# Performance work log

Measured on AMD Instinct MI355X. Metric: run time of the kernel, lower is better.

Reference implementation:

```python
import jax, jax.numpy as jnp
import numpy as np

KERNEL = 7
PAD = 3


def setup_inputs() -> dict:
    key = jax.random.key(0)
    k1, k2, k3 = jax.random.split(key, 3)
    B, C, H, W = 16, 256, 64, 64
    x = jax.random.normal(k1, (B, C, H, W), dtype=jnp.float32)
    weight = jax.random.normal(k2, (C, KERNEL * KERNEL), dtype=jnp.float32)
    bias = jax.random.normal(k3, (C,), dtype=jnp.float32)
    return {"x": x, "weight": weight, "bias": bias}


def reference(x, weight, bias):
    # x: (B, C, H, W); weight: (C, K*K) laid out row-major as in nn.Unfold
    # (unfold * weight).sum over the K*K patch dim == depthwise 'same' conv.
    C = weight.shape[0]
    kernel = weight.reshape(C, 1, KERNEL, KERNEL)  # OIHW with I=1, groups=C
    out = jax.lax.conv_general_dilated(
        x, kernel,
        window_strides=(1, 1),
        padding=((PAD, PAD), (PAD, PAD)),
        dimension_numbers=("NCHW", "OIHW", "NCHW"),
        feature_group_count=C,
    )
    out = out + bias[None, :, None, None]
    # Original wraps this in to_sparse(): a lossless repacking of nonzero
    # pixels into (indices, features) with data-dependent shape. Its dense()
    # equals `out`, so we return the dense form.
    return out
```

## Files before the change

### kernel.cpp

```cpp
#include <hip/hip_runtime.h>

#define LDSW 80
#define LDSH 70
#define KSZ 7
#define PAD 3

__global__ __launch_bounds__(256, 4)
void dwconv7x7_kernel(const float* __restrict__ x,
                      const float* __restrict__ weight,
                      const float* __restrict__ bias,
                      float* __restrict__ out) {
    __shared__ float tile[LDSH * LDSW];

    const int bc  = blockIdx.x;
    const int c   = bc & 255;
    const int tid = threadIdx.x;

    const float4 z4 = make_float4(0.f, 0.f, 0.f, 0.f);
#pragma unroll
    for (int k = 0; k < 6; ++k) {
        int g = tid + k * 256;
        if (g < (LDSH * LDSW) / 4)
            *reinterpret_cast<float4*>(&tile[g * 4]) = z4;
    }

    const float* wp = weight + c * (KSZ * KSZ);
    float wk[KSZ * KSZ];
#pragma unroll
    for (int k = 0; k < KSZ * KSZ; ++k) wk[k] = wp[k];
    const float bv = bias[c];

    __syncthreads();

    const float* xp = x + (size_t)bc * 4096;
#pragma unroll
    for (int k = 0; k < 4; ++k) {
        int g = tid + k * 256;
        int h = g >> 4;
        int w = (g & 15) * 4;
        float4 v = *reinterpret_cast<const float4*>(&xp[g * 4]);
        *reinterpret_cast<float4*>(&tile[(h + PAD) * LDSW + (w + 4)]) = v;
    }
    __syncthreads();

    const int tx = tid & 15;
    const int ty = tid >> 4;
    const int wb = tx * 4;
    const int hb = ty * 4;

    float acc[4][4];
#pragma unroll
    for (int i = 0; i < 4; ++i)
#pragma unroll
        for (int j = 0; j < 4; ++j) acc[i][j] = 0.f;

#pragma unroll
    for (int r = 0; r < 10; ++r) {
        const float* row = &tile[(hb + r) * LDSW + wb];
        float4 q0 = *reinterpret_cast<const float4*>(row);
        float4 q1 = *reinterpret_cast<const float4*>(row + 4);
        float4 q2 = *reinterpret_cast<const float4*>(row + 8);
        float f[12] = {q0.x, q0.y, q0.z, q0.w,
                       q1.x, q1.y, q1.z, q1.w,
                       q2.x, q2.y, q2.z, q2.w};
#pragma unroll
        for (int i = 0; i < 4; ++i) {
            if (r - i >= 0 && r - i <= 6) {
                const int kr = r - i;
#pragma unroll
                for (int j = 0; j < 4; ++j) {
#pragma unroll
                    for (int kc = 0; kc < KSZ; ++kc) {
                        acc[i][j] += f[j + 1 + kc] * wk[kr * KSZ + kc];
                    }
                }
            }
        }
    }

    float* op = out + (size_t)bc * 4096;
#pragma unroll
    for (int i = 0; i < 4; ++i) {
        float4 v;
        v.x = acc[i][0] + bv;
        v.y = acc[i][1] + bv;
        v.z = acc[i][2] + bv;
        v.w = acc[i][3] + bv;
        *reinterpret_cast<float4*>(&op[(hb + i) * 64 + wb]) = v;
    }
}

extern "C" void kernel_launch(void* const* d_in, const int* in_sizes, int n_in,
                              void* d_out, int out_size, void* d_ws, size_t ws_size,
                              hipStream_t stream) {
    const float* x      = (const float*)d_in[0];
    const float* weight = (const float*)d_in[1];
    const float* bias   = (const float*)d_in[2];
    float* out          = (float*)d_out;
    (void)in_sizes; (void)n_in; (void)out_size; (void)d_ws; (void)ws_size;

    dim3 grid(16 * 256);
    dim3 block(256);
    dwconv7x7_kernel<<<grid, block, 0, stream>>>(x, weight, bias, out);
}
```

Before: 39.31 us.

## Replace LDS tiling with direct global loads into registers per wave

Drops the shared-memory tile, its zero-fill and both barriers. Each wave now handles half a plane, and each thread computes an 8x4 output block by reading 14 input rows straight from global memory with float4 loads and masking the padding in registers. This removes LDS traffic and synchronisation and raises output reuse per thread. In exchange it issues redundant global loads that depend on the L1/L2 cache, and needs more registers for the 8x4 accumulators.

```diff
diff --git a/kernel.cpp b/kernel.cpp
--- a/kernel.cpp
+++ b/kernel.cpp
@@ -1,92 +1,91 @@
 #include <hip/hip_runtime.h>
 
-#define LDSW 80
-#define LDSH 70
-#define KSZ 7
-#define PAD 3
 
-__global__ __launch_bounds__(256, 4)
-void dwconv7x7_kernel(const float* __restrict__ x,
-                      const float* __restrict__ weight,
-                      const float* __restrict__ bias,
-                      float* __restrict__ out) {
-    __shared__ float tile[LDSH * LDSW];
+__global__ void dwconv7x7_regs(const float* __restrict__ x,
+                               const float* __restrict__ weight,
+                               const float* __restrict__ bias,
+                               float* __restrict__ out) {
+    const int tid  = threadIdx.x;
+    const int lane = tid & 63;
+    const int wid  = tid >> 6;
+    const int gw   = blockIdx.x * 4 + wid;
+    const int plane = gw >> 1;
+    const int half  = gw & 1;
+    const int c = __builtin_amdgcn_readfirstlane(plane & 255);
 
-    const int bc  = blockIdx.x;
-    const int c   = bc & 255;
-    const int tid = threadIdx.x;
-
-    const float4 z4 = make_float4(0.f, 0.f, 0.f, 0.f);
+    const float* wp = weight + c * 49;
+    float wk[49];
 #pragma unroll
-    for (int k = 0; k < 6; ++k) {
-        int g = tid + k * 256;
-        if (g < (LDSH * LDSW) / 4)
-            *reinterpret_cast<float4*>(&tile[g * 4]) = z4;
-    }
-
-    const float* wp = weight + c * (KSZ * KSZ);
-    float wk[KSZ * KSZ];
-#pragma unroll
-    for (int k = 0; k < KSZ * KSZ; ++k) wk[k] = wp[k];
+    for (int k = 0; k < 49; ++k) wk[k] = wp[k];
     const float bv = bias[c];
 
-    __syncthreads();
+    const int tx = lane & 15;
+    const int sy = lane >> 4;
+    const int wb = tx * 4;
+    const int hb = half * 32 + sy * 8;
 
-    const float* xp = x + (size_t)bc * 4096;
+    const float* xp = x + (size_t)plane * 4096;
+
+    float acc[8][4];
 #pragma unroll
-    for (int k = 0; k < 4; ++k) {
-        int g = tid + k * 256;
-        int h = g >> 4;
-        int w = (g & 15) * 4;
-        float4 v = *reinterpret_cast<const float4*>(&xp[g * 4]);
-        *reinterpret_cast<float4*>(&tile[(h + PAD) * LDSW + (w + 4)]) = v;
-    }
-    __syncthreads();
-
-    const int tx = tid & 15;
-    const int ty = tid >> 4;
-    const int wb = tx * 4;
-    const int hb = ty * 4;
-
-    float acc[4][4];
-#pragma unroll
-    for (int i = 0; i < 4; ++i)
+    for (int i = 0; i < 8; ++i)
 #pragma unroll
         for (int j = 0; j < 4; ++j) acc[i][j] = 0.f;
 
+    const int offm = (tx > 0)  ? (wb - 4) : wb;
+    const int offp = (tx < 15) ? (wb + 4) : wb;
+
 #pragma unroll
-    for (int r = 0; r < 10; ++r) {
-        const float* row = &tile[(hb + r) * LDSW + wb];
-        float4 q0 = *reinterpret_cast<const float4*>(row);
-        float4 q1 = *reinterpret_cast<const float4*>(row + 4);
-        float4 q2 = *reinterpret_cast<const float4*>(row + 8);
-        float f[12] = {q0.x, q0.y, q0.z, q0.w,
-                       q1.x, q1.y, q1.z, q1.w,
-                       q2.x, q2.y, q2.z, q2.w};
+    for (int j = 0; j < 14; ++j) {
+        const int r  = hb - 3 + j;
+        const int rc = min(max(r, 0), 63);
+        const float* rowp = xp + rc * 64;
+        const bool mrow = (r >= 0) && (r < 64);
+        const bool mm = mrow && (tx > 0);
+        const bool mp = mrow && (tx < 15);
+
+        float4 q0 = *reinterpret_cast<const float4*>(rowp + wb);
+        float4 qm = *reinterpret_cast<const float4*>(rowp + offm);
+        float4 qp = *reinterpret_cast<const float4*>(rowp + offp);
+
+        float f[12];
+        f[0]  = mm   ? qm.x : 0.f;
+        f[1]  = mm   ? qm.y : 0.f;
+        f[2]  = mm   ? qm.z : 0.f;
+        f[3]  = mm   ? qm.w : 0.f;
+        f[4]  = mrow ? q0.x : 0.f;
+        f[5]  = mrow ? q0.y : 0.f;
+        f[6]  = mrow ? q0.z : 0.f;
+        f[7]  = mrow ? q0.w : 0.f;
+        f[8]  = mp   ? qp.x : 0.f;
+        f[9]  = mp   ? qp.y : 0.f;
+        f[10] = mp   ? qp.z : 0.f;
+        f[11] = mp   ? qp.w : 0.f;
+
 #pragma unroll
-        for (int i = 0; i < 4; ++i) {
-            if (r - i >= 0 && r - i <= 6) {
-                const int kr = r - i;
+        for (int oi = 0; oi < 8; ++oi) {
+            const int kr = j - oi;
+            if (kr >= 0 && kr < 7) {
 #pragma unroll
-                for (int j = 0; j < 4; ++j) {
+                for (int jj = 0; jj < 4; ++jj) {
 #pragma unroll
-                    for (int kc = 0; kc < KSZ; ++kc) {
-                        acc[i][j] += f[j + 1 + kc] * wk[kr * KSZ + kc];
+                    for (int kc = 0; kc < 7; ++kc) {
+                        acc[oi][jj] += f[1 + jj + kc] * wk[kr * 7 + kc];
                     }
                 }
             }
         }
     }
 
-    float* op = out + (size_t)bc * 4096;
+    float* op = out + (size_t)plane * 4096 + (size_t)hb * 64 + wb;
 #pragma unroll
-    for (int i = 0; i < 4; ++i) {
+    for (int oi = 0; oi < 8; ++oi) {
         float4 v;
-        v.x = acc[i][0] + bv;
-        v.y = acc[i][1] + bv;
-        v.z = acc[i][2] + bv;
-        v.w = acc[i][3] + bv;
-        *reinterpret_cast<float4*>(&op[(hb + i) * 64 + wb]) = v;
+        v.x = acc[oi][0] + bv;
+        v.y = acc[oi][1] + bv;
+        v.z = acc[oi][2] + bv;
+        v.w = acc[oi][3] + bv;
+        *reinterpret_cast<float4*>(op + oi * 64) = v;
     }
 }
 
@@ -99,7 +98,7 @@
     float* out          = (float*)d_out;
     (void)in_sizes; (void)n_in; (void)out_size; (void)d_ws; (void)ws_size;
 
-    dim3 grid(16 * 256);
+    dim3 grid(2048);
     dim3 block(256);
-    dwconv7x7_kernel<<<grid, block, 0, stream>>>(x, weight, bias, out);
+    dwconv7x7_regs<<<grid, block, 0, stream>>>(x, weight, bias, out);
 }
```

Result: faster. 34.81 us (-11.4%).
